# Kernel tuning notes

Measured on AMD Instinct MI355X. Metric: run time of the kernel, lower is better.

Reference implementation:

```python
import jax, jax.numpy as jnp
import numpy as np

B, S, DIM = 2, 2048, 2048
N_HEADS, N_KV_HEADS = 16, 4
HEAD_DIM = DIM // N_HEADS  # 128
N_REP = N_HEADS // N_KV_HEADS
ROPE_THETA = 10000.0


def _rope_cos_sin(bsz, seqlen, head_dim, theta):
    # precompute_freqs_cis (unscaled): angles[t, i] = t * theta^{-2i/d}
    inv_freq = 1.0 / (theta ** (np.arange(0, head_dim, 2)[: head_dim // 2].astype(np.float32) / head_dim))
    t = np.arange(seqlen, dtype=np.float32)
    ang = np.outer(t, inv_freq)  # [S, hd/2]
    cos = np.broadcast_to(np.cos(ang), (bsz, seqlen, head_dim // 2))
    sin = np.broadcast_to(np.sin(ang), (bsz, seqlen, head_dim // 2))
    return jnp.asarray(cos), jnp.asarray(sin)


def setup_inputs() -> dict:
    key = jax.random.key(0)
    ks = jax.random.split(key, 5)
    scale = 1.0 / np.sqrt(DIM)
    x = jax.random.normal(ks[0], (B, S, DIM), dtype=jnp.float32)
    wq = jax.random.normal(ks[1], (DIM, N_HEADS * HEAD_DIM), dtype=jnp.float32) * scale
    wk = jax.random.normal(ks[2], (DIM, N_KV_HEADS * HEAD_DIM), dtype=jnp.float32) * scale
    wv = jax.random.normal(ks[3], (DIM, N_KV_HEADS * HEAD_DIM), dtype=jnp.float32) * scale
    wo = jax.random.normal(ks[4], (N_HEADS * HEAD_DIM, DIM), dtype=jnp.float32) * scale
    freqs_cos, freqs_sin = _rope_cos_sin(B, S, HEAD_DIM, ROPE_THETA)
    return {"x": x, "wq": wq, "wk": wk, "wv": wv, "wo": wo,
            "freqs_cos": freqs_cos, "freqs_sin": freqs_sin}


def _apply_rope(t, cos, sin):
    # t: [B, S, H, hd]; cos/sin: [B, S, hd/2] -> complex mult on (even, odd) pairs
    tr = t.reshape(*t.shape[:-1], -1, 2)  # [B,S,H,hd/2,2]
    xr, xi = tr[..., 0], tr[..., 1]
    c = cos[:, :, None, :]
    s = sin[:, :, None, :]
    out_r = xr * c - xi * s
    out_i = xr * s + xi * c
    return jnp.stack([out_r, out_i], axis=-1).reshape(t.shape)


def reference(x, wq, wk, wv, wo, freqs_cos, freqs_sin):
    bsz, seqlen, _ = x.shape
    xq = (x @ wq).reshape(bsz, seqlen, N_HEADS, HEAD_DIM)
    xk = (x @ wk).reshape(bsz, seqlen, N_KV_HEADS, HEAD_DIM)
    xv = (x @ wv).reshape(bsz, seqlen, N_KV_HEADS, HEAD_DIM)

    xq = _apply_rope(xq, freqs_cos, freqs_sin)
    xk = _apply_rope(xk, freqs_cos, freqs_sin)

    # repeat_kv (GQA): [B,S,KV,hd] -> [B,S,H,hd]
    xk = jnp.repeat(xk, N_REP, axis=2)
    xv = jnp.repeat(xv, N_REP, axis=2)

    # [B,H,Sq,Sk]
    scores = jnp.einsum('bqhd,bkhd->bhqk', xq, xk) / np.sqrt(HEAD_DIM).astype(np.float32)
    # additive causal mask (triu of -inf, diagonal=1)
    causal = jnp.triu(jnp.full((seqlen, seqlen), -jnp.inf, dtype=scores.dtype), k=1)
    scores = scores + causal
    probs = jax.nn.softmax(scores.astype(jnp.float32), axis=-1).astype(xq.dtype)
    out = jnp.einsum('bhqk,bkhd->bqhd', probs, xv).reshape(bsz, seqlen, -1)
    return out @ wo
```

## Files before the change

### kernel.cpp

```cpp
#include <hip/hip_runtime.h>
#include <stdint.h>

#define SEQ   2048
#define NB    2
#define LDQKV 3072
#define HD    128
#define QSCALE2 (0.08838834764831845f * 1.44269504088896340f)

typedef __attribute__((ext_vector_type(8))) short short8;
typedef __attribute__((ext_vector_type(4))) short short4v;
typedef __attribute__((ext_vector_type(4))) float f32x4;
typedef __attribute__((ext_vector_type(16))) float f32x16;
typedef __attribute__((ext_vector_type(4))) unsigned int u32x4;
typedef __attribute__((ext_vector_type(2))) unsigned int u32x2;
typedef __attribute__((ext_vector_type(8))) __bf16 bf16x8;

__device__ __forceinline__ float bs2f(short s) {
  unsigned int u = ((unsigned int)(unsigned short)s) << 16;
  return __builtin_bit_cast(float, u);
}
__device__ __forceinline__ short f2bs(float f) {
  unsigned int u = __builtin_bit_cast(unsigned int, f);
  u += 0x7fffu + ((u >> 16) & 1u);
  return (short)(u >> 16);
}
__device__ __forceinline__ unsigned int cvt_pk(float lo, float hi) {
  unsigned int r;
  asm("v_cvt_pk_bf16_f32 %0, %1, %2" : "=v"(r) : "v"(lo), "v"(hi));
  return r;
}
__device__ __forceinline__ float fexp2(float x) {
  float r;
  asm("v_exp_f32 %0, %1" : "=v"(r) : "v"(x));
  return r;
}
__device__ __forceinline__ f32x4 mfma16(short8 a, short8 b, f32x4 c) {
  return __builtin_amdgcn_mfma_f32_16x16x32_bf16(
      __builtin_bit_cast(bf16x8, a), __builtin_bit_cast(bf16x8, b), c, 0, 0, 0);
}
__device__ __forceinline__ f32x16 mfma32(short8 a, short8 b, f32x16 c) {
  return __builtin_amdgcn_mfma_f32_32x32x16_bf16(
      __builtin_bit_cast(bf16x8, a), __builtin_bit_cast(bf16x8, b), c, 0, 0, 0);
}
__device__ __forceinline__ void gload_lds16(const void* g, void* l) {
  __builtin_amdgcn_global_load_lds(
      (__attribute__((address_space(1))) const void*)(uintptr_t)g,
      (__attribute__((address_space(3))) void*)(unsigned int)(uintptr_t)l,
      16, 0, 0);
}

#define SBAR() asm volatile("s_barrier" ::: "memory")
#define VMC(n) asm volatile("s_waitcnt vmcnt(" #n ")" ::: "memory")

__global__ __launch_bounds__(256) void k_prep(const float* __restrict__ x,
                                              const float* __restrict__ wq,
                                              const float* __restrict__ wk,
                                              const float* __restrict__ wv,
                                              const float* __restrict__ wo,
                                              short* __restrict__ xb,
                                              short* __restrict__ wT,
                                              short* __restrict__ woT) {
  __shared__ __align__(16) float tile[64][68];
  const int bid = blockIdx.x, t = threadIdx.x;
  if (bid < 4096) {
    int i = bid * 256 + t;
    f32x4 a = *(const f32x4*)(x + (size_t)i * 8);
    f32x4 b = *(const f32x4*)(x + (size_t)i * 8 + 4);
    short8 o;
#pragma unroll
    for (int j = 0; j < 4; ++j) { o[j] = f2bs(a[j]); o[4 + j] = f2bs(b[j]); }
    *(short8*)(xb + (size_t)i * 8) = o;
    return;
  }
  const float* src;
  short* dst;
  int N, id;
  if (bid < 5120)      { id = bid - 4096; src = wq; dst = wT;                        N = 2048; }
  else if (bid < 5376) { id = bid - 5120; src = wk; dst = wT + (size_t)2048 * 2048;  N = 512;  }
  else if (bid < 5632) { id = bid - 5376; src = wv; dst = wT + (size_t)2560 * 2048;  N = 512;  }
  else                 { id = bid - 5632; src = wo; dst = woT;                       N = 2048; }
  const int K = 2048;
  int k0 = (id & 31) * 64, n0 = (id >> 5) * 64;
#pragma unroll
  for (int rep = 0; rep < 4; ++rep) {
    int lin = rep * 1024 + t * 4;
    int kk = lin >> 6, nn = lin & 63;
    f32x4 v = *(const f32x4*)(src + (size_t)(k0 + kk) * N + n0 + nn);
    *(f32x4*)(&tile[kk][nn]) = v;
  }
  __syncthreads();
#pragma unroll
  for (int rep = 0; rep < 4; ++rep) {
    int lin = rep * 1024 + t * 4;
    int nn = lin >> 6, kk = lin & 63;
    short4v o;
#pragma unroll
    for (int j = 0; j < 4; ++j) o[j] = f2bs(tile[kk + j][nn]);
    *(short4v*)(dst + (size_t)(n0 + nn) * K + k0 + kk) = o;
  }
}

template <int NH, int FP32OUT, int ROPE>
__global__ __launch_bounds__(512, 2) void k_gemm256(const short* __restrict__ A,
                                                    const short* __restrict__ Bt,
                                                    void* __restrict__ Cp,
                                                    const float* __restrict__ fcos,
                                                    const float* __restrict__ fsin,
                                                    int M, int N, int K) {
  __shared__ short Al[2][2][128 * 64];
  __shared__ short Bl[2][NH][128 * 64];
  const int t = threadIdx.x, l = t & 63, w = t >> 6;
  const int pm = w >> 2, pn = w & 3;
  const int lrow = l & 15, lg = l >> 4;
  const int NT = K >> 6;

  const int nbm = M >> 8;
  const int per = gridDim.x >> 3;
  const int id2 = (blockIdx.x & 7) * per + (blockIdx.x >> 3);
  const int m0 = (id2 % nbm) * 256, n0 = (id2 / nbm) * (NH * 128);

  const int srow = w * 8 + (l >> 3);
  const int sgx = ((l & 7) ^ (srow & 7)) * 8;
  const short* Abase = A + (size_t)(m0 + srow) * K + sgx;
  const short* Bbase = Bt + (size_t)(n0 + srow) * K + sgx;

  f32x4 acc[8][NH * 2] = {};
  short8 aFr0[4][2], aFr1[4][2], bFr[NH][2][2];

  auto stgA = [&](int d, int h, int tv) {
    const short* g = Abase + (size_t)(h * 128) * K + (size_t)tv * 64;
    gload_lds16(g, &Al[d][h][w * 512]);
    gload_lds16(g + (size_t)64 * K, &Al[d][h][w * 512 + 4096]);
  };
  auto stgB = [&](int d, int h, int tv) {
    const short* g = Bbase + (size_t)(h * 128) * K + (size_t)tv * 64;
    gload_lds16(g, &Bl[d][h][w * 512]);
    gload_lds16(g + (size_t)64 * K, &Bl[d][h][w * 512 + 4096]);
  };
  auto rdA = [&](int d, int Mh, short8 (*dst)[2]) {
#pragma unroll
    for (int mi = 0; mi < 4; ++mi) {
      int rl = pm * 64 + mi * 16 + lrow;
#pragma unroll
      for (int kk = 0; kk < 2; ++kk)
        dst[mi][kk] = *(const short8*)&Al[d][Mh][rl * 64 +
                                                 (((kk * 4 + lg) ^ (rl & 7)) * 8)];
    }
  };
  auto rdB = [&](int d) {
#pragma unroll
    for (int h = 0; h < NH; ++h)
#pragma unroll
      for (int ni = 0; ni < 2; ++ni) {
        int rl = pn * 32 + ni * 16 + lrow;
#pragma unroll
        for (int kk = 0; kk < 2; ++kk)
          bFr[h][ni][kk] =
              *(const short8*)&Bl[d][h][rl * 64 +
                                        (((kk * 4 + lg) ^ (rl & 7)) * 8)];
      }
  };

#define MMH(Mh, FR)                                                          \
  do {                                                                       \
    __builtin_amdgcn_s_setprio(1);                                           \
    _Pragma("unroll") for (int h = 0; h < NH; ++h)                           \
        _Pragma("unroll") for (int mi = 0; mi < 4; ++mi)                     \
            _Pragma("unroll") for (int ni = 0; ni < 2; ++ni)                 \
                _Pragma("unroll") for (int kk = 0; kk < 2; ++kk)             \
                    acc[(Mh)*4 + mi][h * 2 + ni] =                           \
                        mfma16(FR[mi][kk], bFr[h][ni][kk],                   \
                               acc[(Mh)*4 + mi][h * 2 + ni]);                \
    __builtin_amdgcn_s_setprio(0);                                           \
  } while (0)

  stgA(0, 0, 0);
  for (int h = 0; h < NH; ++h) stgB(0, h, 0);
  stgA(0, 1, 0);
  stgA(1, 0, 1);
  if (NH == 2) stgB(1, 1, 1);
  if (NH == 2) { VMC(4); } else { VMC(2); }
  SBAR();

  for (int v = 0; v < NT; ++v) {
    const int d = v & 1, d1 = d ^ 1;
    rdA(d, 0, aFr0);
    rdB(d);
    rdA(d, 1, aFr1);
    if (v + 1 < NT) { stgB(d1, 0, v + 1); stgA(d1, 1, v + 1); }
    MMH(0, aFr0);
    SBAR();
    if (v + 2 < NT) {
      stgA(d, 0, v + 2);
      if (NH == 2) stgB(d, 1, v + 2);
    }
    MMH(1, aFr1);
    if (v + 2 < NT) {
      if (NH == 2) { VMC(4); } else { VMC(2); }
    } else {
      VMC(0);
    }
    SBAR();
  }
#undef MMH

#pragma unroll
  for (int Mh = 0; Mh < 2; ++Mh)
#pragma unroll
    for (int mi = 0; mi < 4; ++mi)
#pragma unroll
      for (int h = 0; h < NH; ++h)
#pragma unroll
        for (int ni = 0; ni < 2; ++ni) {
          int row = m0 + Mh * 128 + pm * 64 + mi * 16 + lg * 4;
          int col = n0 + h * 128 + pn * 32 + ni * 16 + lrow;
          f32x4 vv = acc[Mh * 4 + mi][h * 2 + ni];
          if constexpr (ROPE) {
            if (col < 2560) {
              const float qs = (col < 2048) ? QSCALE2 : 1.0f;
              const int p = (col & 127) >> 1;
              const bool ev = ((lrow & 1) == 0);
#pragma unroll
              for (int v2 = 0; v2 < 4; ++v2) {
                float c = fcos[(size_t)(row + v2) * 64 + p] * qs;
                float s = fsin[(size_t)(row + v2) * 64 + p] * qs;
                float xx = vv[v2];
                float xp = __shfl_xor(xx, 1);
                vv[v2] = ev ? (xx * c - xp * s) : (xp * s + xx * c);
              }
            }
          }
#pragma unroll
          for (int v2 = 0; v2 < 4; ++v2) {
            if constexpr (FP32OUT)
              ((float*)Cp)[(size_t)(row + v2) * N + col] = vv[v2];
            else
              ((short*)Cp)[(size_t)(row + v2) * N + col] = f2bs(vv[v2]);
          }
        }
}

__global__ __launch_bounds__(256) void k_vt(const short* __restrict__ qkv,
                                            short* __restrict__ vt) {
  __shared__ short tile[128 * 137];
  const int id = blockIdx.x, t = threadIdx.x;
  int s0 = (id & 15) * 128;
  int kvh = (id >> 4) & 3, b = id >> 6;
  const short* src = qkv + (size_t)(b * SEQ) * LDQKV + 2560 + kvh * 128;
#pragma unroll
  for (int rep = 0; rep < 8; ++rep) {
    int lin = rep * 2048 + t * 8;
    int si = lin >> 7, d = lin & 127;
    short8 v = *(const short8*)(src + (size_t)(s0 + si) * LDQKV + d);
#pragma unroll
    for (int j = 0; j < 8; ++j) tile[si * 137 + d + j] = v[j];
  }
  __syncthreads();
  short* dst = vt + (size_t)((b * 4 + kvh) * 128) * SEQ;
#pragma unroll
  for (int rep = 0; rep < 8; ++rep) {
    int lin = rep * 2048 + t * 8;
    int d = lin >> 7, sb = lin & 127;
    short8 o;
#pragma unroll
    for (int j = 0; j < 8; ++j) o[j] = tile[(sb + j) * 137 + d];
    *(short8*)(dst + (size_t)d * SEQ + s0 + sb) = o;
  }
}

__global__ __launch_bounds__(256, 2) void k_attn(const short* __restrict__ qkv,
                                                 const short* __restrict__ vt,
                                                 short* __restrict__ outp) {
  __shared__ short Ks[2][64 * 128];
  __shared__ short Vs[2][128 * 64];
  const int t = threadIdx.x, l = t & 63, w = t >> 6;
  const int wr = w >> 1, wk = w & 1;
  const int h = blockIdx.y, b = blockIdx.z;
  const int kvh = h >> 2;
  const int lo5 = l & 31, hi = l >> 5;

  const int kkey = t >> 4, kd8 = t & 15;
  const int vdd = t >> 3, vs8 = t & 7;
  const short* kbase = qkv + (size_t)(b * SEQ) * LDQKV + 2048 + kvh * HD;
  const short* vbase = vt + (size_t)((b * 4 + kvh) * 128) * SEQ;

  auto stageKV = [&](int buf, int it) {
    const int kt = it * 64;
    short* kdst = &Ks[buf][w * 512];
    short* vdst = &Vs[buf][w * 512];
#pragma unroll
    for (int i = 0; i < 4; ++i) {
      int key = i * 16 + kkey;
      int sd = (kd8 ^ (key & 15)) * 8;
      gload_lds16(kbase + (size_t)(kt + key) * LDQKV + sd, kdst + i * 2048);
    }
#pragma unroll
    for (int i = 0; i < 4; ++i) {
      int d = i * 32 + vdd;
      int ss = (vs8 ^ (d & 7)) * 8;
      gload_lds16(vbase + (size_t)d * SEQ + kt + ss, vdst + i * 2048);
    }
  };

  int koff[8], voff[4][2];
#pragma unroll
  for (int s = 0; s < 8; ++s)
    koff[s] = (wk * 32 + lo5) * 128 + (((hi + 2 * s) ^ (l & 15)) * 8);
#pragma unroll
  for (int db = 0; db < 4; ++db)
#pragma unroll
    for (int s = 0; s < 2; ++s)
      voff[db][s] =
          (db * 32 + lo5) * 64 + (((4 * wk + hi + 2 * s) ^ (l & 7)) * 8);
  const int kbloc = wk * 32 + 4 * hi;
  const int qloc = wr * 32 + lo5;

  for (int part = 0; part < 2; ++part) {
    const int qt = part ? (31 - (int)blockIdx.x) : (int)blockIdx.x;
    const int q0 = qt * 64;

    short8 qf[8];
    {
      const short* qrow =
          qkv + (size_t)(b * SEQ + q0 + wr * 32 + lo5) * LDQKV + h * HD;
#pragma unroll
      for (int s = 0; s < 8; ++s)
        qf[s] = *(const short8*)(qrow + s * 16 + hi * 8);
    }

    f32x16 of[4] = {};
    float mrun = 0.f, lsum = 0.f;

    const int nt = qt + 1;
    stageKV(0, 0);
    __syncthreads();

    for (int it = 0; it < nt; ++it) {
      const int buf = it & 1;
      if (it + 1 < nt) stageKV(buf ^ 1, it + 1);
      const short* KsC = Ks[buf];
      const short* VsC = Vs[buf];

      f32x16 sca = {}, scb = {};
      __builtin_amdgcn_s_setprio(1);
#pragma unroll
      for (int s = 0; s < 4; ++s) {
        short8 kf0 = *(const short8*)(KsC + koff[2 * s]);
        short8 kf1 = *(const short8*)(KsC + koff[2 * s + 1]);
        sca = mfma32(kf0, qf[2 * s], sca);
        scb = mfma32(kf1, qf[2 * s + 1], scb);
      }
      __builtin_amdgcn_s_setprio(0);
      f32x16 sc = sca + scb;

      if (it == nt - 1) {
#pragma unroll
        for (int r = 0; r < 16; ++r) {
          const int off = (r & 3) + 8 * (r >> 2);
          if (kbloc + off > qloc) sc[r] = -1e30f;
        }
      }

      float lmax = sc[0];
#pragma unroll
      for (int r = 1; r < 16; ++r) lmax = fmaxf(lmax, sc[r]);
      if (__any(lmax > mrun + 8.f)) {
        float mx = fmaxf(lmax, __shfl_xor(lmax, 32));
        float mm = fmaxf(mrun, mx);
        float rs = fexp2(mrun - mm);
        mrun = mm;
        lsum *= rs;
#pragma unroll
        for (int db = 0; db < 4; ++db)
#pragma unroll
          for (int r = 0; r < 16; ++r) of[db][r] *= rs;
      }

      float p[16];
#pragma unroll
      for (int r = 0; r < 16; ++r) {
        p[r] = fexp2(sc[r] - mrun);
        lsum += p[r];
      }
      unsigned int pk[8];
#pragma unroll
      for (int j = 0; j < 8; ++j) pk[j] = cvt_pk(p[2 * j], p[2 * j + 1]);

      unsigned int s0 = hi ? pk[0] : pk[2];
      unsigned int s1 = hi ? pk[1] : pk[3];
      unsigned int s2 = hi ? pk[4] : pk[6];
      unsigned int s3 = hi ? pk[5] : pk[7];
      unsigned int x0 = __shfl_xor(s0, 32);
      unsigned int x1 = __shfl_xor(s1, 32);
      unsigned int x2 = __shfl_xor(s2, 32);
      unsigned int x3 = __shfl_xor(s3, 32);
      u32x4 b0w, b1w;
      b0w.x = hi ? x0 : pk[0];
      b0w.y = hi ? x1 : pk[1];
      b0w.z = hi ? pk[2] : x0;
      b0w.w = hi ? pk[3] : x1;
      b1w.x = hi ? x2 : pk[4];
      b1w.y = hi ? x3 : pk[5];
      b1w.z = hi ? pk[6] : x2;
      b1w.w = hi ? pk[7] : x3;
      short8 pb[2] = {__builtin_bit_cast(short8, b0w),
                      __builtin_bit_cast(short8, b1w)};

      __builtin_amdgcn_s_setprio(1);
#pragma unroll
      for (int s = 0; s < 2; ++s)
#pragma unroll
        for (int db = 0; db < 4; ++db) {
          short8 vf = *(const short8*)(VsC + voff[db][s]);
          of[db] = mfma32(vf, pb[s], of[db]);
        }
      __builtin_amdgcn_s_setprio(0);
      __syncthreads();
    }

    lsum += __shfl_xor(lsum, 32);
    float* og = (float*)Ks;
    float* sg = (float*)Vs;
    if (wk == 1) {
#pragma unroll
      for (int db = 0; db < 4; ++db)
#pragma unroll
        for (int r4 = 0; r4 < 4; ++r4) {
          int g = db * 4 + r4;
          f32x4 v;
#pragma unroll
          for (int j = 0; j < 4; ++j) v[j] = of[db][r4 * 4 + j];
          *(f32x4*)&og[wr * 4096 + l * 64 + ((g ^ (l & 15)) * 4)] = v;
        }
      sg[wr * 64 + l] = mrun;
      sg[128 + wr * 64 + l] = lsum;
    }
    __syncthreads();
    if (wk == 0) {
      float m1 = sg[wr * 64 + l];
      float l1 = sg[128 + wr * 64 + l];
      float mt = fmaxf(mrun, m1);
      float r0 = fexp2(mrun - mt), r1 = fexp2(m1 - mt);
      float inv = 1.0f / (lsum * r0 + l1 * r1);
      short* ob =
          outp + (size_t)(b * SEQ + q0 + wr * 32 + lo5) * 2048 + h * HD;
#pragma unroll
      for (int db = 0; db < 4; ++db) {
#pragma unroll
        for (int r4 = 0; r4 < 4; ++r4) {
          int g = db * 4 + r4;
          f32x4 o1 = *(const f32x4*)&og[wr * 4096 + l * 64 +
                                        ((g ^ (l & 15)) * 4)];
          u32x2 pko;
          float v0 = (of[db][r4 * 4 + 0] * r0 + o1[0] * r1) * inv;
          float v1 = (of[db][r4 * 4 + 1] * r0 + o1[1] * r1) * inv;
          float v2 = (of[db][r4 * 4 + 2] * r0 + o1[2] * r1) * inv;
          float v3 = (of[db][r4 * 4 + 3] * r0 + o1[3] * r1) * inv;
          pko.x = cvt_pk(v0, v1);
          pko.y = cvt_pk(v2, v3);
          *(u32x2*)(ob + db * 32 + 8 * r4 + 4 * hi) = pko;
        }
      }
    }
    __syncthreads();
  }
}

extern "C" void kernel_launch(void* const* d_in, const int* in_sizes, int n_in,
                              void* d_out, int out_size, void* d_ws,
                              size_t ws_size, hipStream_t stream) {
  const float* x = (const float*)d_in[0];
  const float* wq = (const float*)d_in[1];
  const float* wk = (const float*)d_in[2];
  const float* wv = (const float*)d_in[3];
  const float* wo = (const float*)d_in[4];
  const float* fc = (const float*)d_in[5];
  const float* fs = (const float*)d_in[6];

  char* ws = (char*)d_ws;
  short* xb = (short*)(ws);
  short* wT = (short*)(ws + (16ull << 20));
  short* woT = (short*)(ws + (28ull << 20));
  short* qkvb = (short*)(ws + (36ull << 20));
  short* vtb = (short*)(ws + (16ull << 20));
  short* attn = (short*)(ws);

  k_prep<<<6656, 256, 0, stream>>>(x, wq, wk, wv, wo, xb, wT, woT);
  k_gemm256<2, 0, 1><<<192, 512, 0, stream>>>(xb, wT, qkvb, fc, fs,
                                              4096, 3072, 2048);
  k_vt<<<128, 256, 0, stream>>>(qkvb, vtb);
  k_attn<<<dim3(16, 16, 2), 256, 0, stream>>>(qkvb, vtb, attn);
  k_gemm256<1, 1, 0><<<256, 512, 0, stream>>>(attn, woT, d_out, nullptr,
                                              nullptr, 4096, 2048, 2048);
}
```

Measured before the change: 183.1 us.

## Split GEMM main loop into quarter-tile MFMA phases with per-half B reads

Restructures the double-buffered GEMM main loop so B fragments are read from LDS one N-half at a time and the MFMA work is issued in four quarter blocks (M-half by N-half) with barriers between them. Global-to-LDS staging is interleaved between the quarters, aiming to shorten register live ranges and overlap loads with compute more evenly. The RoPE epilogue also hoists cos/sin loads out of the head loop and computes the scale per tile rather than per column. The extra barriers add synchronisation cost per iteration.

```diff
diff --git a/kernel.cpp b/kernel.cpp
--- a/kernel.cpp
+++ b/kernel.cpp
@@ -147,30 +147,27 @@
                                                  (((kk * 4 + lg) ^ (rl & 7)) * 8)];
     }
   };
-  auto rdB = [&](int d) {
-#pragma unroll
-    for (int h = 0; h < NH; ++h)
-#pragma unroll
-      for (int ni = 0; ni < 2; ++ni) {
-        int rl = pn * 32 + ni * 16 + lrow;
-#pragma unroll
-        for (int kk = 0; kk < 2; ++kk)
-          bFr[h][ni][kk] =
-              *(const short8*)&Bl[d][h][rl * 64 +
-                                        (((kk * 4 + lg) ^ (rl & 7)) * 8)];
-      }
+  auto rdBh = [&](int d, int h) {
+#pragma unroll
+    for (int ni = 0; ni < 2; ++ni) {
+      int rl = pn * 32 + ni * 16 + lrow;
+#pragma unroll
+      for (int kk = 0; kk < 2; ++kk)
+        bFr[h][ni][kk] =
+            *(const short8*)&Bl[d][h][rl * 64 +
+                                      (((kk * 4 + lg) ^ (rl & 7)) * 8)];
+    }
   };
 
-#define MMH(Mh, FR)                                                          \
+#define MMQ(Mh, Nh, FR)                                                      \
   do {                                                                       \
     __builtin_amdgcn_s_setprio(1);                                           \
-    _Pragma("unroll") for (int h = 0; h < NH; ++h)                           \
-        _Pragma("unroll") for (int mi = 0; mi < 4; ++mi)                     \
-            _Pragma("unroll") for (int ni = 0; ni < 2; ++ni)                 \
-                _Pragma("unroll") for (int kk = 0; kk < 2; ++kk)             \
-                    acc[(Mh)*4 + mi][h * 2 + ni] =                           \
-                        mfma16(FR[mi][kk], bFr[h][ni][kk],                   \
-                               acc[(Mh)*4 + mi][h * 2 + ni]);                \
+    _Pragma("unroll") for (int mi = 0; mi < 4; ++mi)                         \
+        _Pragma("unroll") for (int ni = 0; ni < 2; ++ni)                     \
+            _Pragma("unroll") for (int kk = 0; kk < 2; ++kk)                 \
+                acc[(Mh)*4 + mi][(Nh)*2 + ni] =                              \
+                    mfma16(FR[mi][kk], bFr[Nh][ni][kk],                      \
+                           acc[(Mh)*4 + mi][(Nh)*2 + ni]);                   \
     __builtin_amdgcn_s_setprio(0);                                           \
   } while (0)
 
@@ -185,49 +182,72 @@
   for (int v = 0; v < NT; ++v) {
     const int d = v & 1, d1 = d ^ 1;
     rdA(d, 0, aFr0);
-    rdB(d);
+    rdBh(d, 0);
+    if (v + 1 < NT) {
+      stgB(d1, 0, v + 1);
+      if (NH == 1) stgA(d1, 1, v + 1);
+    }
+    SBAR();
+    MMQ(0, 0, aFr0);
+    SBAR();
+    if (NH == 2) {
+      rdBh(d, 1);
+      if (v + 1 < NT) stgA(d1, 1, v + 1);
+      SBAR();
+      MMQ(0, 1, aFr0);
+      SBAR();
+    }
     rdA(d, 1, aFr1);
-    if (v + 1 < NT) { stgB(d1, 0, v + 1); stgA(d1, 1, v + 1); }
-    MMH(0, aFr0);
+    if (v + 2 < NT) stgA(d, 0, v + 2);
     SBAR();
-    if (v + 2 < NT) {
-      stgA(d, 0, v + 2);
-      if (NH == 2) stgB(d, 1, v + 2);
-    }
-    MMH(1, aFr1);
-    if (v + 2 < NT) {
-      if (NH == 2) { VMC(4); } else { VMC(2); }
+    if (NH == 2) {
+      MMQ(1, 1, aFr1);
+      SBAR();
+      if (v + 2 < NT) stgB(d, 1, v + 2);
+      SBAR();
+      MMQ(1, 0, aFr1);
+      if (v + 2 < NT) { VMC(4); } else { VMC(0); }
+      SBAR();
     } else {
-      VMC(0);
-    }
-    SBAR();
-  }
-#undef MMH
-
+      MMQ(1, 0, aFr1);
+      if (v + 2 < NT) { VMC(2); } else { VMC(0); }
+      SBAR();
+    }
+  }
+#undef MMQ
+
+  const bool doRope = ROPE && (n0 < 2560);
+  const float qs = (n0 < 2048) ? QSCALE2 : 1.0f;
+  const int p0i = (pn * 32 + lrow) >> 1;
+  const bool ev = ((lrow & 1) == 0);
 #pragma unroll
   for (int Mh = 0; Mh < 2; ++Mh)
 #pragma unroll
-    for (int mi = 0; mi < 4; ++mi)
+    for (int mi = 0; mi < 4; ++mi) {
+      const int row = m0 + Mh * 128 + pm * 64 + mi * 16 + lg * 4;
+      float cc[4][2], ss[4][2];
+      if (doRope) {
+#pragma unroll
+        for (int v2 = 0; v2 < 4; ++v2)
+#pragma unroll
+          for (int ni = 0; ni < 2; ++ni) {
+            cc[v2][ni] = fcos[(size_t)(row + v2) * 64 + p0i + ni * 8] * qs;
+            ss[v2][ni] = fsin[(size_t)(row + v2) * 64 + p0i + ni * 8] * qs;
+          }
+      }
 #pragma unroll
       for (int h = 0; h < NH; ++h)
 #pragma unroll
         for (int ni = 0; ni < 2; ++ni) {
-          int row = m0 + Mh * 128 + pm * 64 + mi * 16 + lg * 4;
           int col = n0 + h * 128 + pn * 32 + ni * 16 + lrow;
           f32x4 vv = acc[Mh * 4 + mi][h * 2 + ni];
-          if constexpr (ROPE) {
-            if (col < 2560) {
-              const float qs = (col < 2048) ? QSCALE2 : 1.0f;
-              const int p = (col & 127) >> 1;
-              const bool ev = ((lrow & 1) == 0);
-#pragma unroll
-              for (int v2 = 0; v2 < 4; ++v2) {
-                float c = fcos[(size_t)(row + v2) * 64 + p] * qs;
-                float s = fsin[(size_t)(row + v2) * 64 + p] * qs;
-                float xx = vv[v2];
-                float xp = __shfl_xor(xx, 1);
-                vv[v2] = ev ? (xx * c - xp * s) : (xp * s + xx * c);
-              }
+          if (doRope) {
+#pragma unroll
+            for (int v2 = 0; v2 < 4; ++v2) {
+              float xx = vv[v2];
+              float xp = __shfl_xor(xx, 1);
+              vv[v2] = ev ? (xx * cc[v2][ni] - xp * ss[v2][ni])
+                          : (xp * ss[v2][ni] + xx * cc[v2][ni]);
             }
           }
 #pragma unroll
@@ -238,6 +258,7 @@
               ((short*)Cp)[(size_t)(row + v2) * N + col] = f2bs(vv[v2]);
           }
         }
+    }
 }
 
 __global__ __launch_bounds__(256) void k_vt(const short* __restrict__ qkv,
```

Result: no change. 184.4 us (+0.7%).
